# Performance work log

Measured on AMD Instinct MI355X. Metric: run time of the kernel, lower is better.

Reference implementation:

```python
import jax, jax.numpy as jnp
import numpy as np

N_NODES = 50000
N_EDGES = 800000
N_GRAPHS = 8
IN_CH = 32
HID = 64
EDGE_F = 16
EPS = 1e-5


def setup_inputs() -> dict:
    key = jax.random.key(0)
    ks = jax.random.split(key, 40)
    r = lambda i, shape, s=0.1: (jax.random.normal(ks[i], shape, dtype=jnp.float32) * s)
    inp = {
        "x": jax.random.normal(ks[0], (N_NODES, IN_CH), dtype=jnp.float32),
        "edge_index": jax.random.randint(ks[1], (2, N_EDGES), 0, N_NODES),
        "edge_attr": jax.random.normal(ks[2], (N_EDGES, EDGE_F), dtype=jnp.float32),
        "batch": jnp.sort(jax.random.randint(ks[3], (N_NODES,), 0, N_GRAPHS)),
        "nt_w": r(4, (IN_CH, HID)), "nt_b": jnp.zeros((HID,), jnp.float32),
        "ln0_w": jnp.ones((HID,), jnp.float32), "ln0_b": jnp.zeros((HID,), jnp.float32),
        "c1_wl": r(5, (HID, 2 * HID)), "c1_bl": jnp.zeros((2 * HID,), jnp.float32),
        "c1_wr": r(6, (HID, 2 * HID)), "c1_br": jnp.zeros((2 * HID,), jnp.float32),
        "c1_we": r(7, (EDGE_F, 2 * HID)), "c1_att": r(8, (2, HID)),
        "c1_b": jnp.zeros((2 * HID,), jnp.float32),
        "n1_w": jnp.ones((2 * HID,), jnp.float32), "n1_b": jnp.zeros((2 * HID,), jnp.float32),
        "c2_wl": r(9, (2 * HID, 2 * HID)), "c2_bl": jnp.zeros((2 * HID,), jnp.float32),
        "c2_wr": r(10, (2 * HID, 2 * HID)), "c2_br": jnp.zeros((2 * HID,), jnp.float32),
        "c2_we": r(11, (EDGE_F, 2 * HID)), "c2_att": r(12, (2, HID)),
        "c2_b": jnp.zeros((2 * HID,), jnp.float32),
        "n2_w": jnp.ones((2 * HID,), jnp.float32), "n2_b": jnp.zeros((2 * HID,), jnp.float32),
        "c3_wl": r(13, (2 * HID, HID)), "c3_bl": jnp.zeros((HID,), jnp.float32),
        "c3_wr": r(14, (2 * HID, HID)), "c3_br": jnp.zeros((HID,), jnp.float32),
        "c3_we": r(15, (EDGE_F, HID)), "c3_att": r(16, (1, HID)),
        "c3_b": jnp.zeros((HID,), jnp.float32),
        "pof_w": r(17, (HID, 1)), "pof_b": jnp.zeros((1,), jnp.float32),
        "hp_w": r(18, (HID, 1)), "hp_b": jnp.zeros((1,), jnp.float32),
    }
    return inp


def _layer_norm(x, w, b):
    # torch nn.LayerNorm over last dim
    mu = jnp.mean(x, axis=-1, keepdims=True)
    xc = x - mu
    var = jnp.mean(xc * xc, axis=-1, keepdims=True)
    return xc * jax.lax.rsqrt(var + EPS) * w + b


def _graph_norm(x, w, b):
    # PyG LayerNorm mode='graph' with batch=None: normalize over all nodes+channels
    mu = jnp.mean(x)
    xc = x - mu
    var = jnp.mean(xc * xc)
    return xc * jax.lax.rsqrt(var + EPS) * w + b


def _gatv2(x, src, dst, ea, wl, bl, wr, br, we, att, b, heads, outc):
    n = x.shape[0]
    xl = (x @ wl + bl).reshape(n, heads, outc)   # source transform
    xr = (x @ wr + br).reshape(n, heads, outc)   # target transform
    e = (ea @ we).reshape(-1, heads, outc)       # [E,H,C] edge embedding
    m = jax.nn.leaky_relu(xl[src] + xr[dst] + e, 0.2)  # [E,H,C]
    alpha = jnp.einsum("ehc,hc->eh", m, att)      # [E,H]
    amax = jax.ops.segment_max(alpha, dst, num_segments=n)
    amax = jnp.where(jnp.isfinite(amax), amax, 0.0)
    p = jnp.exp(alpha - amax[dst])
    denom = jax.ops.segment_sum(p, dst, num_segments=n)
    alpha = p / (denom[dst] + 1e-16)
    out = jax.ops.segment_sum(xl[src] * alpha[..., None], dst, num_segments=n)
    return out.reshape(n, heads * outc) + b


def reference(x, edge_index, edge_attr, batch,
              nt_w, nt_b, ln0_w, ln0_b,
              c1_wl, c1_bl, c1_wr, c1_br, c1_we, c1_att, c1_b, n1_w, n1_b,
              c2_wl, c2_bl, c2_wr, c2_br, c2_we, c2_att, c2_b, n2_w, n2_b,
              c3_wl, c3_bl, c3_wr, c3_br, c3_we, c3_att, c3_b,
              pof_w, pof_b, hp_w, hp_b):
    src, dst = edge_index[0], edge_index[1]
    # node_transform (dropout = identity in eval mode)
    h = _layer_norm(jax.nn.elu(x @ nt_w + nt_b), ln0_w, ln0_b)
    h = _gatv2(h, src, dst, edge_attr, c1_wl, c1_bl, c1_wr, c1_br, c1_we, c1_att, c1_b, 2, HID)
    h = jax.nn.elu(_graph_norm(h, n1_w, n1_b))
    h = _gatv2(h, src, dst, edge_attr, c2_wl, c2_bl, c2_wr, c2_br, c2_we, c2_att, c2_b, 2, HID)
    h = jax.nn.elu(_graph_norm(h, n2_w, n2_b))
    h = _gatv2(h, src, dst, edge_attr, c3_wl, c3_bl, c3_wr, c3_br, c3_we, c3_att, c3_b, 1, HID)
    pof_pred = (h @ pof_w + pof_b)[:, 0]
    sums = jax.ops.segment_sum(h, batch, num_segments=N_GRAPHS)
    cnt = jax.ops.segment_sum(jnp.ones((h.shape[0],), h.dtype), batch, num_segments=N_GRAPHS)
    graph_emb = sums / jnp.maximum(cnt, 1.0)[:, None]
    has_pof_pred = (graph_emb @ hp_w + hp_b)[:, 0]
    return pof_pred, has_pof_pred
```

## Files before the change

kernel.cpp:

```cpp
#include <hip/hip_runtime.h>
#include <cstdint>
#include <cstddef>

#define DI __device__ __forceinline__

constexpr int N = 50000;
constexpr int E = 800000;
constexpr int NG = 8;

constexpr size_t AL(size_t x){ return (x + 1023) & ~size_t(1023); }
constexpr size_t OFF_SCAL   = 0;
constexpr size_t OFF_GSUM   = 1024;
constexpr size_t OFF_GCNT   = OFF_GSUM + 2048;
constexpr size_t OFF_DEG    = 4096;
constexpr size_t ZERO_BYTES = OFF_DEG + size_t(N)*4;
constexpr size_t OFF_ROWPTR = AL(ZERO_BYTES);
constexpr size_t OFF_CURSOR = AL(OFF_ROWPTR + size_t(N+1)*4);
constexpr size_t OFF_BSUM   = AL(OFF_CURSOR + size_t(N)*4);
constexpr size_t OFF_BOFF   = AL(OFF_BSUM + 1024);
constexpr size_t OFF_COLSRC = AL(OFF_BOFF + 1024);
constexpr size_t OFF_COLDST = AL(OFF_COLSRC + size_t(E)*4);
constexpr size_t OFF_EAC    = AL(OFF_COLDST + size_t(E)*4);
constexpr size_t OFF_BL     = AL(OFF_EAC + size_t(E)*32);
constexpr size_t OFF_BR     = AL(OFF_BL + size_t(N)*64*4);
constexpr size_t OFF_A      = AL(OFF_BR + size_t(N)*64*4);
constexpr size_t OFF_CACC   = AL(OFF_A + size_t(N)*64*4);
constexpr size_t OFF_DACC   = AL(OFF_CACC + size_t(N)*128*4);
constexpr size_t CACC_ZERO  = (OFF_DACC - OFF_CACC) + size_t(N)*2*4;

template<int START>
DI float wred(float v){
  #pragma unroll
  for (int o = START; o > 0; o >>= 1) v += __shfl_xor(v, o);
  return v;
}

DI float elu(float v){ return v > 0.f ? v : (__expf(v) - 1.f); }

typedef __attribute__((ext_vector_type(2))) __fp16 h2v;

DI uint32_t pkh(float a, float b){
  auto r = __builtin_amdgcn_cvt_pkrtz(a, b);
  return __builtin_bit_cast(uint32_t, r);
}
DI float hlo(uint32_t u){ h2v h = __builtin_bit_cast(h2v, u); return (float)h.x; }
DI float hhi(uint32_t u){ h2v h = __builtin_bit_cast(h2v, u); return (float)h.y; }
DI float h2f(uint16_t u){ __fp16 h = __builtin_bit_cast(__fp16, u); return (float)h; }

#if __has_builtin(__builtin_amdgcn_fdot2)
DI float dot2(uint32_t a, uint32_t b, float c){
  return __builtin_amdgcn_fdot2(__builtin_bit_cast(h2v, a),
                                __builtin_bit_cast(h2v, b), c, false);
}
#else
DI float dot2(uint32_t a, uint32_t b, float c){
  return fmaf(hlo(a), hlo(b), fmaf(hhi(a), hhi(b), c));
}
#endif

__global__ void k_deg(const int* __restrict__ ei, int* __restrict__ deg){
  for (int e = blockIdx.x*blockDim.x + threadIdx.x; e < E; e += gridDim.x*blockDim.x)
    atomicAdd(&deg[ei[E + e]], 1);
}

__global__ __launch_bounds__(256) void k_scan1(const int* __restrict__ deg,
                                               int* __restrict__ rowptr,
                                               int* __restrict__ bsum){
  __shared__ int s[256];
  int t = threadIdx.x, i = blockIdx.x*256 + t;
  int v = (i < N) ? deg[i] : 0;
  s[t] = v; __syncthreads();
  for (int off = 1; off < 256; off <<= 1){
    int x = (t >= off) ? s[t-off] : 0;
    __syncthreads();
    s[t] += x; __syncthreads();
  }
  if (i < N) rowptr[i] = s[t] - v;
  if (t == 255) bsum[blockIdx.x] = s[255];
}

__global__ __launch_bounds__(256) void k_scan2(const int* __restrict__ bsum,
                                               int* __restrict__ boff, int nb){
  __shared__ int s[256];
  int t = threadIdx.x;
  int v = (t < nb) ? bsum[t] : 0;
  s[t] = v; __syncthreads();
  for (int off = 1; off < 256; off <<= 1){
    int x = (t >= off) ? s[t-off] : 0;
    __syncthreads();
    s[t] += x; __syncthreads();
  }
  if (t < nb) boff[t] = s[t] - v;
}

__global__ __launch_bounds__(256) void k_scan3(int* __restrict__ rowptr,
                                               const int* __restrict__ boff,
                                               int* __restrict__ cursor){
  int t = threadIdx.x, i = blockIdx.x*256 + t;
  if (i < N){
    int v = rowptr[i] + boff[blockIdx.x];
    rowptr[i] = v;
    cursor[i] = v;
  }
  if (i == 0) rowptr[N] = E;
}

__global__ void k_fill(const int* __restrict__ ei, const float* __restrict__ ea,
                       int* __restrict__ cursor, int* __restrict__ colsrc,
                       int* __restrict__ coldst, uint32_t* __restrict__ eac){
  for (int e = blockIdx.x*blockDim.x + threadIdx.x; e < E; e += gridDim.x*blockDim.x){
    int dn = ei[E + e];
    int pos = atomicAdd(&cursor[dn], 1);
    colsrc[pos] = ei[e];
    coldst[pos] = dn;
    const float4* s = (const float4*)(ea + size_t(e)*16);
    float4 v0 = s[0], v1 = s[1], v2 = s[2], v3 = s[3];
    uint32_t* d8 = eac + size_t(pos)*8;
    d8[0] = pkh(v0.x, v0.y); d8[1] = pkh(v0.z, v0.w);
    d8[2] = pkh(v1.x, v1.y); d8[3] = pkh(v1.z, v1.w);
    d8[4] = pkh(v2.x, v2.y); d8[5] = pkh(v2.z, v2.w);
    d8[6] = pkh(v3.x, v3.y); d8[7] = pkh(v3.z, v3.w);
  }
}

__global__ __launch_bounds__(256) void k_node_transform(
    const float* __restrict__ x, const float* __restrict__ w,
    const float* __restrict__ b, const float* __restrict__ lnw,
    const float* __restrict__ lnb, uint32_t* __restrict__ A){
  int wid = (blockIdx.x*256 + threadIdx.x) >> 6;
  int l = threadIdx.x & 63;
  if (wid >= N) return;
  float xv = x[wid*32 + (l & 31)];
  float acc = b[l];
  #pragma unroll
  for (int k = 0; k < 32; ++k){
    float hk = __shfl(xv, k);
    acc = fmaf(hk, w[k*64 + l], acc);
  }
  float v = elu(acc);
  float mu = wred<32>(v) * (1.f/64.f);
  float xc = v - mu;
  float var = wred<32>(xc*xc) * (1.f/64.f);
  float rs = rsqrtf(var + 1e-5f);
  float o = xc*rs*lnw[l] + lnb[l];
  float partner = __shfl_xor(o, 1);
  if ((l & 1) == 0) A[wid*32 + (l >> 1)] = pkh(o, partner);
}

template<int K, int C>
__global__ __launch_bounds__(256) void k_lin2(
    const uint32_t* __restrict__ h,
    const float* __restrict__ Wl_, const float* __restrict__ bl_,
    const float* __restrict__ Wr_, const float* __restrict__ br_,
    uint32_t* __restrict__ Bl, uint32_t* __restrict__ Br){
  constexpr int CB = 64;
  constexpr int NL = C / CB;
  constexpr int NCB = 2*NL;
  constexpr int NT = 32;
  constexpr int WQ = K / 4;
  __shared__ float Wl[K][CB];
  __shared__ float Hl[NT][K + 4];
  const int tid = threadIdx.x;
  const int cb = blockIdx.x % NCB;
  const int tile0 = blockIdx.x / NCB;
  const int tstep = gridDim.x / NCB;
  const bool left = cb < NL;
  const float* W = left ? Wl_ : Wr_;
  const float* bias = left ? bl_ : br_;
  uint32_t* Out = left ? Bl : Br;
  const int wcb = left ? cb : cb - NL;
  for (int idx = tid; idx < K*CB; idx += 256){
    int k = idx >> 6, c = idx & 63;
    Wl[k][c] = W[k*C + wcb*CB + c];
  }
  const int nl = tid >> 4;
  const int cq = tid & 15;
  const float* bb = bias + wcb*CB + cq*4;
  float4 b4 = make_float4(bb[0], bb[1], bb[2], bb[3]);
  constexpr int NTILES = (N + NT - 1)/NT;
  for (int tile = tile0; tile < NTILES; tile += tstep){
    int n0 = tile*NT;
    __syncthreads();
    for (int idx = tid; idx < NT*WQ; idx += 256){
      int nn = idx / WQ, q = idx % WQ;
      uint2 v = make_uint2(0,0);
      int n = n0 + nn;
      if (n < N) v = ((const uint2*)(h + size_t(n)*(K/2)))[q];
      Hl[nn][4*q]   = hlo(v.x);
      Hl[nn][4*q+1] = hhi(v.x);
      Hl[nn][4*q+2] = hlo(v.y);
      Hl[nn][4*q+3] = hhi(v.y);
    }
    __syncthreads();
    float4 a0 = make_float4(0,0,0,0), a1 = a0;
    #pragma unroll 8
    for (int k = 0; k < K; ++k){
      float4 w4 = ((const float4*)&Wl[k][0])[cq];
      float h0v = Hl[nl][k];
      float h1v = Hl[nl+16][k];
      a0.x = fmaf(h0v, w4.x, a0.x); a0.y = fmaf(h0v, w4.y, a0.y);
      a0.z = fmaf(h0v, w4.z, a0.z); a0.w = fmaf(h0v, w4.w, a0.w);
      a1.x = fmaf(h1v, w4.x, a1.x); a1.y = fmaf(h1v, w4.y, a1.y);
      a1.z = fmaf(h1v, w4.z, a1.z); a1.w = fmaf(h1v, w4.w, a1.w);
    }
    int na = n0 + nl, nb2 = n0 + nl + 16;
    if (na < N){
      uint2 o = make_uint2(pkh(a0.x+b4.x, a0.y+b4.y), pkh(a0.z+b4.z, a0.w+b4.w));
      ((uint2*)(Out + size_t(na)*(C/2)))[wcb*16 + cq] = o;
    }
    if (nb2 < N){
      uint2 o = make_uint2(pkh(a1.x+b4.x, a1.y+b4.y), pkh(a1.z+b4.z, a1.w+b4.w));
      ((uint2*)(Out + size_t(nb2)*(C/2)))[wcb*16 + cq] = o;
    }
  }
}

DI float edge_logit2(float xlx, float xly, float xrx, float xry,
                     const uint32_t* wp0, const uint32_t* wp1, float2 at2,
                     uint4 qa, uint4 qb){
  float c0 = xlx + xrx, c1 = xly + xry;
  uint32_t wq[8] = {qa.x,qa.y,qa.z,qa.w, qb.x,qb.y,qb.z,qb.w};
  #pragma unroll
  for (int k = 0; k < 8; ++k){
    c0 = dot2(wq[k], wp0[k], c0);
    c1 = dot2(wq[k], wp1[k], c1);
  }
  c0 = c0 > 0.f ? c0 : 0.2f*c0;
  c1 = c1 > 0.f ? c1 : 0.2f*c1;
  return wred<16>(c0*at2.x + c1*at2.y);
}

DI float edge_logit1(float xl, float xr, const uint32_t* wp, float at,
                     uint4 qa, uint4 qb){
  float c0 = xl + xr;
  uint32_t wq[8] = {qa.x,qa.y,qa.z,qa.w, qb.x,qb.y,qb.z,qb.w};
  #pragma unroll
  for (int k = 0; k < 8; ++k) c0 = dot2(wq[k], wp[k], c0);
  c0 = c0 > 0.f ? c0 : 0.2f*c0;
  return wred<32>(c0*at);
}

constexpr int CHUNK = 32;
constexpr int NCHUNK = E / CHUNK;

template<int H>
__global__ __launch_bounds__(256, 6) void k_attagg(
    const uint32_t* __restrict__ Bl, const uint32_t* __restrict__ Br,
    const float* __restrict__ we, const float* __restrict__ att,
    const uint32_t* __restrict__ eac,
    const int* __restrict__ colsrc, const int* __restrict__ coldst,
    float* __restrict__ Cacc, float* __restrict__ Dacc){
  const int tid = threadIdx.x;
  const int l = tid & 63;
  const int g = (blockIdx.x*256 + tid) >> 6;
  if (g >= NCHUNK) return;
  const int e0 = g*CHUNK;
  const uint4* eb = (const uint4*)eac;
  const int cs = colsrc[e0 + (l & 31)];
  const int cd = coldst[e0 + (l & 31)];
  if constexpr (H == 2){
    uint32_t wp0[8], wp1[8];
    #pragma unroll
    for (int k = 0; k < 8; ++k){
      wp0[k] = pkh(we[(2*k)*128 + 2*l],   we[(2*k+1)*128 + 2*l]);
      wp1[k] = pkh(we[(2*k)*128 + 2*l+1], we[(2*k+1)*128 + 2*l+1]);
    }
    const float2 at2 = ((const float2*)att)[l];
    int cur = __shfl(cd, 0);
    uint32_t xrw = Br[size_t(cur)*64 + l];
    float xrx = hlo(xrw), xry = hhi(xrw);
    float d = 0.f, a0 = 0.f, a1 = 0.f;
    #pragma unroll 1
    for (int jb = 0; jb < CHUNK; jb += 4){
      int s0 = __shfl(cs, jb),   s1 = __shfl(cs, jb+1);
      int s2 = __shfl(cs, jb+2), s3 = __shfl(cs, jb+3);
      uint32_t x0 = Bl[size_t(s0)*64 + l];
      uint32_t x1 = Bl[size_t(s1)*64 + l];
      uint32_t x2 = Bl[size_t(s2)*64 + l];
      uint32_t x3 = Bl[size_t(s3)*64 + l];
      const uint4* q = eb + size_t(e0 + jb)*2;
      uint4 qa0 = q[0], qb0 = q[1], qa1 = q[2], qb1 = q[3];
      uint4 qa2 = q[4], qb2 = q[5], qa3 = q[6], qb3 = q[7];
      int d0 = __shfl(cd, jb),   d1 = __shfl(cd, jb+1);
      int d2 = __shfl(cd, jb+2), d3 = __shfl(cd, jb+3);
      #define FLUSH2(dn) { \
        atomicAdd(&Cacc[size_t(cur)*128 + 2*l],   a0); \
        atomicAdd(&Cacc[size_t(cur)*128 + 2*l+1], a1); \
        if (l == 0)  atomicAdd(&Dacc[cur*2],   d); \
        if (l == 32) atomicAdd(&Dacc[cur*2+1], d); \
        cur = dn; xrw = Br[size_t(cur)*64 + l]; \
        xrx = hlo(xrw); xry = hhi(xrw); d = a0 = a1 = 0.f; }
      #define EDGE2(xk, qak, qbk) { \
        float t = edge_logit2(hlo(xk), hhi(xk), xrx, xry, wp0, wp1, at2, qak, qbk); \
        float p = __expf(t); d += p; \
        a0 = fmaf(p, hlo(xk), a0); a1 = fmaf(p, hhi(xk), a1); }
      if (d0 != cur) FLUSH2(d0); EDGE2(x0, qa0, qb0);
      if (d1 != cur) FLUSH2(d1); EDGE2(x1, qa1, qb1);
      if (d2 != cur) FLUSH2(d2); EDGE2(x2, qa2, qb2);
      if (d3 != cur) FLUSH2(d3); EDGE2(x3, qa3, qb3);
      #undef FLUSH2
      #undef EDGE2
    }
    atomicAdd(&Cacc[size_t(cur)*128 + 2*l],   a0);
    atomicAdd(&Cacc[size_t(cur)*128 + 2*l+1], a1);
    if (l == 0)  atomicAdd(&Dacc[cur*2],   d);
    if (l == 32) atomicAdd(&Dacc[cur*2+1], d);
  } else {
    uint32_t wp[8];
    #pragma unroll
    for (int k = 0; k < 8; ++k)
      wp[k] = pkh(we[(2*k)*64 + l], we[(2*k+1)*64 + l]);
    const float at = att[l];
    const uint16_t* Bl16 = (const uint16_t*)Bl;
    const uint16_t* Br16 = (const uint16_t*)Br;
    int cur = __shfl(cd, 0);
    float xr = h2f(Br16[size_t(cur)*64 + l]);
    float d = 0.f, a0 = 0.f;
    #pragma unroll 1
    for (int jb = 0; jb < CHUNK; jb += 4){
      int s0 = __shfl(cs, jb),   s1 = __shfl(cs, jb+1);
      int s2 = __shfl(cs, jb+2), s3 = __shfl(cs, jb+3);
      float x0 = h2f(Bl16[size_t(s0)*64 + l]);
      float x1 = h2f(Bl16[size_t(s1)*64 + l]);
      float x2 = h2f(Bl16[size_t(s2)*64 + l]);
      float x3 = h2f(Bl16[size_t(s3)*64 + l]);
      const uint4* q = eb + size_t(e0 + jb)*2;
      uint4 qa0 = q[0], qb0 = q[1], qa1 = q[2], qb1 = q[3];
      uint4 qa2 = q[4], qb2 = q[5], qa3 = q[6], qb3 = q[7];
      int d0 = __shfl(cd, jb),   d1 = __shfl(cd, jb+1);
      int d2 = __shfl(cd, jb+2), d3 = __shfl(cd, jb+3);
      #define FLUSH1(dn) { \
        atomicAdd(&Cacc[size_t(cur)*64 + l], a0); \
        if (l == 0) atomicAdd(&Dacc[cur], d); \
        cur = dn; xr = h2f(Br16[size_t(cur)*64 + l]); d = a0 = 0.f; }
      #define EDGE1(xk, qak, qbk) { \
        float t = edge_logit1(xk, xr, wp, at, qak, qbk); \
        float p = __expf(t); d += p; a0 = fmaf(p, xk, a0); }
      if (d0 != cur) FLUSH1(d0); EDGE1(x0, qa0, qb0);
      if (d1 != cur) FLUSH1(d1); EDGE1(x1, qa1, qb1);
      if (d2 != cur) FLUSH1(d2); EDGE1(x2, qa2, qb2);
      if (d3 != cur) FLUSH1(d3); EDGE1(x3, qa3, qb3);
      #undef FLUSH1
      #undef EDGE1
    }
    atomicAdd(&Cacc[size_t(cur)*64 + l], a0);
    if (l == 0) atomicAdd(&Dacc[cur], d);
  }
}

template<bool GN>
__global__ __launch_bounds__(256) void k_finish2(
    const float* __restrict__ Cacc, const float* __restrict__ Dacc,
    const float* __restrict__ bias, uint32_t* __restrict__ A,
    double* __restrict__ scal){
  float s1p = 0.f, s2p = 0.f;
  for (int i = blockIdx.x*256 + threadIdx.x; i < N*64; i += gridDim.x*256){
    int n = i >> 6, w = i & 63;
    float inv = 1.f/(Dacc[n*2 + (w >> 5)] + 1e-16f);
    float o0 = Cacc[size_t(n)*128 + 2*w]   * inv + bias[2*w];
    float o1 = Cacc[size_t(n)*128 + 2*w+1] * inv + bias[2*w+1];
    A[i] = pkh(o0, o1);
    if constexpr (GN){ s1p += o0 + o1; s2p += o0*o0 + o1*o1; }
  }
  if constexpr (GN){
    float s = wred<32>(s1p), s2 = wred<32>(s2p);
    __shared__ float bs[4], bs2[4];
    int w = threadIdx.x >> 6;
    if ((threadIdx.x & 63) == 0){ bs[w] = s; bs2[w] = s2; }
    __syncthreads();
    if (threadIdx.x == 0){
      double ts  = (double)bs[0] + (double)bs[1] + (double)bs[2] + (double)bs[3];
      double ts2 = (double)bs2[0] + (double)bs2[1] + (double)bs2[2] + (double)bs2[3];
      atomicAdd(&scal[0], ts);
      atomicAdd(&scal[1], ts2);
    }
  }
}

__global__ __launch_bounds__(256) void k_finish1(
    float* __restrict__ Cacc, const float* __restrict__ Dacc,
    const float* __restrict__ bias){
  int i = blockIdx.x*256 + threadIdx.x;
  if (i < N*64){
    int n = i >> 6, c = i & 63;
    Cacc[i] = Cacc[i]/(Dacc[n] + 1e-16f) + bias[c];
  }
}

__global__ __launch_bounds__(256) void k_gn_apply(
    uint32_t* __restrict__ A, const double* __restrict__ scal,
    const float* __restrict__ w, const float* __restrict__ b){
  const double invM = 1.0 / (double(N)*128.0);
  double mu_d = scal[0]*invM;
  double ex2  = scal[1]*invM;
  float mu = (float)mu_d;
  float var = (float)(ex2 - mu_d*mu_d);
  float rs = rsqrtf(var + 1e-5f);
  int i = blockIdx.x*256 + threadIdx.x;
  if (i < N*64){
    int wo = i & 63;
    float2 wv = ((const float2*)w)[wo];
    float2 bv = ((const float2*)b)[wo];
    uint32_t u = A[i];
    float o0 = elu((hlo(u) - mu)*rs*wv.x + bv.x);
    float o1 = elu((hhi(u) - mu)*rs*wv.y + bv.y);
    A[i] = pkh(o0, o1);
  }
}

__global__ __launch_bounds__(256) void k_pool(
    const float* __restrict__ h3, const int* __restrict__ batch,
    const float* __restrict__ pw, const float* __restrict__ pb,
    float* __restrict__ outv, float* __restrict__ gsum, float* __restrict__ gcnt){
  __shared__ float ls[512];
  __shared__ float lc[8];
  int tid = threadIdx.x;
  if (tid < 8) lc[tid] = 0.f;
  for (int i = tid; i < 512; i += 256) ls[i] = 0.f;
  __syncthreads();
  int l = tid & 63;
  int wid = (blockIdx.x*256 + tid) >> 6;
  int NW = (gridDim.x*256) >> 6;
  float pwl = pw[l];
  for (int n = wid; n < N; n += NW){
    float v = h3[size_t(n)*64 + l];
    float pp = wred<32>(v*pwl);
    if (l == 0) outv[n] = pp + pb[0];
    int g = batch[n];
    atomicAdd(&ls[g*64 + l], v);
    if (l == 0) atomicAdd(&lc[g], 1.f);
  }
  __syncthreads();
  for (int i = tid; i < 512; i += 256) atomicAdd(&gsum[i], ls[i]);
  if (tid < 8) atomicAdd(&gcnt[tid], lc[tid]);
}

__global__ __launch_bounds__(512) void k_head(
    const float* __restrict__ gsum, const float* __restrict__ gcnt,
    const float* __restrict__ hw, const float* __restrict__ hb,
    float* __restrict__ outv){
  int g = threadIdx.x >> 6, l = threadIdx.x & 63;
  float cnt = fmaxf(gcnt[g], 1.f);
  float emb = gsum[g*64 + l] / cnt;
  float p = wred<32>(emb*hw[l]);
  if (l == 0) outv[N + g] = p + hb[0];
}

extern "C" void kernel_launch(void* const* d_in, const int* in_sizes, int n_in,
                              void* d_out, int out_size, void* d_ws, size_t ws_size,
                              hipStream_t stream){
  const float* x      = (const float*)d_in[0];
  const int*   ei     = (const int*)  d_in[1];
  const float* ea     = (const float*)d_in[2];
  const int*   batch  = (const int*)  d_in[3];
  const float* nt_w   = (const float*)d_in[4];
  const float* nt_b   = (const float*)d_in[5];
  const float* ln0_w  = (const float*)d_in[6];
  const float* ln0_b  = (const float*)d_in[7];
  const float* c1_wl  = (const float*)d_in[8];
  const float* c1_bl  = (const float*)d_in[9];
  const float* c1_wr  = (const float*)d_in[10];
  const float* c1_br  = (const float*)d_in[11];
  const float* c1_we  = (const float*)d_in[12];
  const float* c1_att = (const float*)d_in[13];
  const float* c1_b   = (const float*)d_in[14];
  const float* n1_w   = (const float*)d_in[15];
  const float* n1_b   = (const float*)d_in[16];
  const float* c2_wl  = (const float*)d_in[17];
  const float* c2_bl  = (const float*)d_in[18];
  const float* c2_wr  = (const float*)d_in[19];
  const float* c2_br  = (const float*)d_in[20];
  const float* c2_we  = (const float*)d_in[21];
  const float* c2_att = (const float*)d_in[22];
  const float* c2_b   = (const float*)d_in[23];
  const float* n2_w   = (const float*)d_in[24];
  const float* n2_b   = (const float*)d_in[25];
  const float* c3_wl  = (const float*)d_in[26];
  const float* c3_bl  = (const float*)d_in[27];
  const float* c3_wr  = (const float*)d_in[28];
  const float* c3_br  = (const float*)d_in[29];
  const float* c3_we  = (const float*)d_in[30];
  const float* c3_att = (const float*)d_in[31];
  const float* c3_b   = (const float*)d_in[32];
  const float* pof_w  = (const float*)d_in[33];
  const float* pof_b  = (const float*)d_in[34];
  const float* hp_w   = (const float*)d_in[35];
  const float* hp_b   = (const float*)d_in[36];
  float* out = (float*)d_out;

  char* w = (char*)d_ws;
  double* scal    = (double*)(w + OFF_SCAL);
  float* gsum     = (float*)(w + OFF_GSUM);
  float* gcnt     = (float*)(w + OFF_GCNT);
  int* deg        = (int*)(w + OFF_DEG);
  int* rowptr     = (int*)(w + OFF_ROWPTR);
  int* cursor     = (int*)(w + OFF_CURSOR);
  int* bsum       = (int*)(w + OFF_BSUM);
  int* boff       = (int*)(w + OFF_BOFF);
  int* colsrc     = (int*)(w + OFF_COLSRC);
  int* coldst     = (int*)(w + OFF_COLDST);
  uint32_t* eac   = (uint32_t*)(w + OFF_EAC);
  uint32_t* Bl    = (uint32_t*)(w + OFF_BL);
  uint32_t* Br    = (uint32_t*)(w + OFF_BR);
  uint32_t* A     = (uint32_t*)(w + OFF_A);
  float* Cacc     = (float*)(w + OFF_CACC);
  float* Dacc     = (float*)(w + OFF_DACC);

  hipMemsetAsync(d_ws, 0, ZERO_BYTES, stream);

  k_deg  <<<1024, 256, 0, stream>>>(ei, deg);
  k_scan1<<<196,  256, 0, stream>>>(deg, rowptr, bsum);
  k_scan2<<<1,    256, 0, stream>>>(bsum, boff, 196);
  k_scan3<<<196,  256, 0, stream>>>(rowptr, boff, cursor);
  k_fill <<<1024, 256, 0, stream>>>(ei, ea, cursor, colsrc, coldst, eac);

  k_node_transform<<<12500, 256, 0, stream>>>(x, nt_w, nt_b, ln0_w, ln0_b, A);

  hipMemsetAsync(w + OFF_CACC, 0, CACC_ZERO, stream);
  k_lin2<64,128><<<2048, 256, 0, stream>>>(A, c1_wl, c1_bl, c1_wr, c1_br, Bl, Br);
  k_attagg<2><<<6250, 256, 0, stream>>>(Bl, Br, c1_we, c1_att, eac, colsrc, coldst, Cacc, Dacc);
  k_finish2<true><<<608, 256, 0, stream>>>(Cacc, Dacc, c1_b, A, scal);
  k_gn_apply<<<12500, 256, 0, stream>>>(A, scal, n1_w, n1_b);

  hipMemsetAsync(w + OFF_CACC, 0, CACC_ZERO, stream);
  k_lin2<128,128><<<2048, 256, 0, stream>>>(A, c2_wl, c2_bl, c2_wr, c2_br, Bl, Br);
  k_attagg<2><<<6250, 256, 0, stream>>>(Bl, Br, c2_we, c2_att, eac, colsrc, coldst, Cacc, Dacc);
  k_finish2<true><<<608, 256, 0, stream>>>(Cacc, Dacc, c2_b, A, scal + 2);
  k_gn_apply<<<12500, 256, 0, stream>>>(A, scal + 2, n2_w, n2_b);

  hipMemsetAsync(w + OFF_CACC, 0, CACC_ZERO, stream);
  k_lin2<128,64><<<1024, 256, 0, stream>>>(A, c3_wl, c3_bl, c3_wr, c3_br, Bl, Br);
  k_attagg<1><<<6250, 256, 0, stream>>>(Bl, Br, c3_we, c3_att, eac, colsrc, coldst, Cacc, Dacc);
  k_finish1<<<12500, 256, 0, stream>>>(Cacc, Dacc, c3_b);

  k_pool<<<512, 256, 0, stream>>>(Cacc, batch, pof_w, pof_b, out, gsum, gcnt);
  k_head<<<1, 512, 0, stream>>>(gsum, gcnt, hp_w, hp_b, out);
}
```

Before: 661.3 us.

## Use packed half dot2 in linear kernel, fuse final normalization into pool

The node linear kernel now keeps weights and node features packed as half pairs in shared memory and accumulates with dot2 instructions. This halves shared-memory traffic and FMA count per output. The final per-node normalization kernel is removed and its divide-plus-bias is folded into the pooling kernel, saving one full pass over the accumulator. The attention-aggregation kernel's launch bound is raised to 8 waves per SIMD, which limits registers and may cause spills; the weights also lose precision by being rounded to half.

```diff
diff --git a/kernel.cpp b/kernel.cpp
--- a/kernel.cpp
+++ b/kernel.cpp
@@ -157,9 +157,10 @@
   constexpr int NL = C / CB;
   constexpr int NCB = 2*NL;
   constexpr int NT = 32;
-  constexpr int WQ = K / 4;
-  __shared__ float Wl[K][CB];
-  __shared__ float Hl[NT][K + 4];
+  constexpr int KQ = K/2;
+  constexpr int WQ2 = K/4;
+  __shared__ uint32_t Wp[KQ][CB];
+  __shared__ uint32_t Hp[NT][KQ + 2];
   const int tid = threadIdx.x;
   const int cb = blockIdx.x % NCB;
   const int tile0 = blockIdx.x / NCB;
@@ -169,9 +170,9 @@
   const float* bias = left ? bl_ : br_;
   uint32_t* Out = left ? Bl : Br;
   const int wcb = left ? cb : cb - NL;
-  for (int idx = tid; idx < K*CB; idx += 256){
-    int k = idx >> 6, c = idx & 63;
-    Wl[k][c] = W[k*C + wcb*CB + c];
+  for (int idx = tid; idx < KQ*CB; idx += 256){
+    int kq = idx >> 6, c = idx & 63;
+    Wp[kq][c] = pkh(W[(2*kq)*C + wcb*CB + c], W[(2*kq+1)*C + wcb*CB + c]);
   }
   const int nl = tid >> 4;
   const int cq = tid & 15;
@@ -181,27 +182,25 @@
   for (int tile = tile0; tile < NTILES; tile += tstep){
     int n0 = tile*NT;
     __syncthreads();
-    for (int idx = tid; idx < NT*WQ; idx += 256){
-      int nn = idx / WQ, q = idx % WQ;
+    for (int idx = tid; idx < NT*WQ2; idx += 256){
+      int nn = idx / WQ2, q = idx % WQ2;
       uint2 v = make_uint2(0,0);
       int n = n0 + nn;
-      if (n < N) v = ((const uint2*)(h + size_t(n)*(K/2)))[q];
-      Hl[nn][4*q]   = hlo(v.x);
-      Hl[nn][4*q+1] = hhi(v.x);
-      Hl[nn][4*q+2] = hlo(v.y);
-      Hl[nn][4*q+3] = hhi(v.y);
+      if (n < N) v = ((const uint2*)(h + size_t(n)*KQ))[q];
+      Hp[nn][2*q]   = v.x;
+      Hp[nn][2*q+1] = v.y;
     }
     __syncthreads();
     float4 a0 = make_float4(0,0,0,0), a1 = a0;
     #pragma unroll 8
-    for (int k = 0; k < K; ++k){
-      float4 w4 = ((const float4*)&Wl[k][0])[cq];
-      float h0v = Hl[nl][k];
-      float h1v = Hl[nl+16][k];
-      a0.x = fmaf(h0v, w4.x, a0.x); a0.y = fmaf(h0v, w4.y, a0.y);
-      a0.z = fmaf(h0v, w4.z, a0.z); a0.w = fmaf(h0v, w4.w, a0.w);
-      a1.x = fmaf(h1v, w4.x, a1.x); a1.y = fmaf(h1v, w4.y, a1.y);
-      a1.z = fmaf(h1v, w4.z, a1.z); a1.w = fmaf(h1v, w4.w, a1.w);
+    for (int kq = 0; kq < KQ; ++kq){
+      uint4 w4 = ((const uint4*)&Wp[kq][0])[cq];
+      uint32_t h0 = Hp[nl][kq];
+      uint32_t h1 = Hp[nl+16][kq];
+      a0.x = dot2(h0, w4.x, a0.x); a0.y = dot2(h0, w4.y, a0.y);
+      a0.z = dot2(h0, w4.z, a0.z); a0.w = dot2(h0, w4.w, a0.w);
+      a1.x = dot2(h1, w4.x, a1.x); a1.y = dot2(h1, w4.y, a1.y);
+      a1.z = dot2(h1, w4.z, a1.z); a1.w = dot2(h1, w4.w, a1.w);
     }
     int na = n0 + nl, nb2 = n0 + nl + 16;
     if (na < N){
@@ -244,7 +243,7 @@
 constexpr int NCHUNK = E / CHUNK;
 
 template<int H>
-__global__ __launch_bounds__(256, 6) void k_attagg(
+__global__ __launch_bounds__(256, 8) void k_attagg(
     const uint32_t* __restrict__ Bl, const uint32_t* __restrict__ Br,
     const float* __restrict__ we, const float* __restrict__ att,
     const uint32_t* __restrict__ eac,
@@ -377,16 +376,6 @@
   }
 }
 
-__global__ __launch_bounds__(256) void k_finish1(
-    float* __restrict__ Cacc, const float* __restrict__ Dacc,
-    const float* __restrict__ bias){
-  int i = blockIdx.x*256 + threadIdx.x;
-  if (i < N*64){
-    int n = i >> 6, c = i & 63;
-    Cacc[i] = Cacc[i]/(Dacc[n] + 1e-16f) + bias[c];
-  }
-}
-
 __global__ __launch_bounds__(256) void k_gn_apply(
     uint32_t* __restrict__ A, const double* __restrict__ scal,
     const float* __restrict__ w, const float* __restrict__ b){
@@ -409,7 +398,8 @@
 }
 
 __global__ __launch_bounds__(256) void k_pool(
-    const float* __restrict__ h3, const int* __restrict__ batch,
+    const float* __restrict__ Cacc, const float* __restrict__ Dacc,
+    const int* __restrict__ batch, const float* __restrict__ bias3,
     const float* __restrict__ pw, const float* __restrict__ pb,
     float* __restrict__ outv, float* __restrict__ gsum, float* __restrict__ gcnt){
   __shared__ float ls[512];
@@ -422,8 +412,9 @@
   int wid = (blockIdx.x*256 + tid) >> 6;
   int NW = (gridDim.x*256) >> 6;
   float pwl = pw[l];
+  float b3 = bias3[l];
   for (int n = wid; n < N; n += NW){
-    float v = h3[size_t(n)*64 + l];
+    float v = Cacc[size_t(n)*64 + l]/(Dacc[n] + 1e-16f) + b3;
     float pp = wred<32>(v*pwl);
     if (l == 0) outv[n] = pp + pb[0];
     int g = batch[n];
@@ -531,8 +522,7 @@
   hipMemsetAsync(w + OFF_CACC, 0, CACC_ZERO, stream);
   k_lin2<128,64><<<1024, 256, 0, stream>>>(A, c3_wl, c3_bl, c3_wr, c3_br, Bl, Br);
   k_attagg<1><<<6250, 256, 0, stream>>>(Bl, Br, c3_we, c3_att, eac, colsrc, coldst, Cacc, Dacc);
-  k_finish1<<<12500, 256, 0, stream>>>(Cacc, Dacc, c3_b);
-
-  k_pool<<<512, 256, 0, stream>>>(Cacc, batch, pof_w, pof_b, out, gsum, gcnt);
+
+  k_pool<<<512, 256, 0, stream>>>(Cacc, Dacc, batch, c3_b, pof_w, pof_b, out, gsum, gcnt);
   k_head<<<1, 512, 0, stream>>>(gsum, gcnt, hp_w, hp_b, out);
 }
```

Result: slower. 945.9 us (+43.0%).
